# Performance work log

Hardware: AMD Instinct MI355X
Metric: run time of the kernel (lower is better)

The kernel has to match this reference:

```python
import jax, jax.numpy as jnp
import numpy as np

N_NODES = 100000
N_EDGES = 1600000
STATE_DIM = 128
HIDDEN_DIM = 128
ACTION_DIM = 16


def gcn_conv(x, edge_index, W, b, n_nodes):
    """PyG-style GCNConv: add self-loops, symmetric normalization, x@W then aggregate."""
    xw = x @ W  # [N, H]
    loops = jnp.arange(n_nodes, dtype=edge_index.dtype)
    src = jnp.concatenate([edge_index[0], loops])  # [E+N]
    dst = jnp.concatenate([edge_index[1], loops])
    ones = jnp.ones(src.shape[0], dtype=xw.dtype)
    deg = jax.ops.segment_sum(ones, dst, num_segments=n_nodes)  # degree of target nodes
    dinv = jnp.where(deg > 0, jax.lax.rsqrt(deg), 0.0)
    norm = dinv[src] * dinv[dst]  # [E+N]
    msg = xw[src] * norm[:, None]  # gather + scale (irregular access)
    out = jax.ops.segment_sum(msg, dst, num_segments=n_nodes)  # scatter-aggregate
    return out + b


def setup_inputs() -> dict:
    key = jax.random.key(0)
    ks = jax.random.split(key, 12)
    def lin(k, fan_in, shape):
        bound = 1.0 / np.sqrt(fan_in)
        return jax.random.uniform(k, shape, jnp.float32, -bound, bound)
    return {
        "x": jax.random.normal(ks[0], (N_NODES, STATE_DIM), jnp.float32),
        "edge_index": jax.random.randint(ks[1], (2, N_EDGES), 0, N_NODES, jnp.int64),
        "action": jax.random.normal(ks[2], (N_NODES, ACTION_DIM), jnp.float32),
        "gcn1_w": lin(ks[3], STATE_DIM, (STATE_DIM, HIDDEN_DIM)),
        "gcn1_b": lin(ks[4], STATE_DIM, (HIDDEN_DIM,)),
        "gcn2_w": lin(ks[5], HIDDEN_DIM, (HIDDEN_DIM, HIDDEN_DIM)),
        "gcn2_b": lin(ks[6], HIDDEN_DIM, (HIDDEN_DIM,)),
        "fc1_w": lin(ks[7], HIDDEN_DIM + ACTION_DIM, (HIDDEN_DIM + ACTION_DIM, HIDDEN_DIM)),
        "fc1_b": lin(ks[8], HIDDEN_DIM + ACTION_DIM, (HIDDEN_DIM,)),
        "fc2_w": lin(ks[9], HIDDEN_DIM, (HIDDEN_DIM, 1)),
        "fc2_b": lin(ks[10], HIDDEN_DIM, (1,)),
    }


def reference(x, edge_index, action, gcn1_w, gcn1_b, gcn2_w, gcn2_b, fc1_w, fc1_b, fc2_w, fc2_b):
    n = x.shape[0]
    h = jax.nn.relu(gcn_conv(x, edge_index, gcn1_w, gcn1_b, n))
    h = jax.nn.relu(gcn_conv(h, edge_index, gcn2_w, gcn2_b, n))
    h = jnp.concatenate([h, action], axis=-1)  # [N, H+A]
    h = jax.nn.relu(h @ fc1_w + fc1_b)
    q = h @ fc2_w + fc2_b  # [N, 1]
    return q.squeeze(-1)
```

## Files before the change

### kernel.cpp

```cpp
#include <hip/hip_runtime.h>
#include <hip/hip_bf16.h>

typedef unsigned short u16;
typedef unsigned int   u32;
typedef __attribute__((ext_vector_type(8))) short bf16x8;
typedef __attribute__((ext_vector_type(4))) float f32x4;

constexpr int NN = 100000;
constexpr int NE = 1600000;
constexpr int D  = 128;
constexpr size_t WS_NEED = 58909184;

constexpr int NBUCK = 196;
constexpr int NBLKA = 256;
constexpr int EPB   = 6272;
constexpr int CAPA  = 80;

__device__ __forceinline__ float bf2f(u16 u){ union{u32 i;float f;}v; v.i=((u32)u)<<16; return v.f; }
__device__ __forceinline__ float2 bfp(u32 u){ union{u32 i;float f;}a,b; a.i=u<<16; b.i=u&0xffff0000u; return make_float2(a.f,b.f); }
__device__ __forceinline__ u16 f2bf(float f){ union{float f;u32 i;}v; v.f=f; u32 r=v.i + 0x7fffu + ((v.i>>16)&1u); return (u16)(r>>16); }
__device__ __forceinline__ u32 pk2(float a, float b){ return (u32)f2bf(a) | ((u32)f2bf(b)<<16); }

__global__ void detect_kernel(const u32* __restrict__ xw, const int* __restrict__ ei,
                              int* __restrict__ flagf, int* __restrict__ flage){
  __shared__ int shf[256];
  __shared__ int she[256];
  int t = threadIdx.x;
  int cnt = 0;
  for(int i = 0; i < 16; i++){
    u32 w = xw[(t*16 + i) * 256];
    int e = (int)((w >> 7) & 0xFFu);
    cnt += (e >= 64 && e <= 160) ? 1 : 0;
  }
  int nz = 0;
  for(int i = 0; i < 8; i++){
    int k = t*8 + i;
    long long w = 1 + ((long long)k * (2LL*NE - 2)) / 2048;
    nz += (ei[(int)(w | 1)] != 0) ? 1 : 0;
  }
  shf[t] = cnt; she[t] = nz;
  __syncthreads();
  for(int off=128; off>0; off>>=1){
    if(t<off){ shf[t]+=shf[t+off]; she[t]+=she[t+off]; }
    __syncthreads();
  }
  if(t==0){ flagf[0] = (shf[0] < 3000) ? 1 : 0; flage[0] = (she[0] == 0) ? 1 : 0; }
}

__global__ void prep_kernel(const void* __restrict__ w1, const void* __restrict__ w2,
    const void* __restrict__ fw1, const void* __restrict__ b1, const void* __restrict__ b2,
    const void* __restrict__ fb1, const void* __restrict__ fw2, const void* __restrict__ fb2,
    const int* __restrict__ flagf,
    u16* __restrict__ WT1, u16* __restrict__ WT2, u16* __restrict__ WTF, float* __restrict__ BF)
{
  const int ff = flagf[0];
  int i = blockIdx.x*256 + threadIdx.x;
  auto cv = [&](const void* p, int idx)->float{
    return ff ? ((const float*)p)[idx] : bf2f(((const u16*)p)[idx]);
  };
  if(i < 16384){
    int k = i >> 7, d = i & 127;
    WT1[d*128 + k] = f2bf(cv(w1, i));
  }else if(i < 32768){
    int j = i - 16384; int k = j >> 7, d = j & 127;
    WT2[d*128 + k] = f2bf(cv(w2, j));
  }else if(i < 51200){
    int j = i - 32768; int k = j >> 7, d = j & 127;
    WTF[d*144 + k] = f2bf(cv(fw1, j));
  }else if(i < 51713){
    int j = i - 51200;
    if(j < 128)       BF[j]   = cv(b1, j);
    else if(j < 256)  BF[j]   = cv(b2, j-128);
    else if(j < 384)  BF[j]   = cv(fb1, j-256);
    else if(j < 512)  BF[j]   = cv(fw2, j-384);
    else              BF[512] = cv(fb2, 0);
  }
}

__global__ void fill1_kernel(u16* __restrict__ out, int n){
  int i = blockIdx.x*blockDim.x + threadIdx.x;
  if(i < n) out[i] = 0x3F80;
}

__global__ __launch_bounds__(256) void passA_kernel(
    const int* __restrict__ ei, const int* __restrict__ flage,
    u32* __restrict__ ebuf, u32* __restrict__ counts)
{
  __shared__ u32 hist[NBUCK];
  int t = threadIdx.x;
  for(int b = t; b < NBUCK; b += 256) hist[b] = 0;
  __syncthreads();
  const int f = flage[0];
  const int eb = blockIdx.x * EPB;
  const u32 cbase = blockIdx.x * NBUCK;
  for(int i = t; i < EPB; i += 256){
    int e = eb + i;
    if(e >= NE) break;
    int s = f ? ei[2*e]      : ei[e];
    int d = f ? ei[2*(NE+e)] : ei[NE+e];
    if((u32)s >= (u32)NN || (u32)d >= (u32)NN) continue;
    int b = d >> 9;
    u32 rank = atomicAdd(&hist[b], 1u);
    if(rank < CAPA) ebuf[(size_t)(cbase + b)*CAPA + rank] = (u32)s | ((u32)(d & 511) << 17);
  }
  __syncthreads();
  for(int b = t; b < NBUCK; b += 256){
    u32 c = hist[b];
    counts[cbase + b] = (c < CAPA) ? c : CAPA;
  }
}

__global__ void scan196_kernel(const u32* __restrict__ counts, int* __restrict__ bases){
  __shared__ int sh[NBUCK];
  int t = threadIdx.x;
  if(t < NBUCK){
    int tot = 0;
    for(int c = 0; c < NBLKA; c++) tot += counts[c*NBUCK + t];
    sh[t] = tot;
  }
  __syncthreads();
  if(t == 0){
    int acc = 0;
    for(int b = 0; b < NBUCK; b++){ int v = sh[b]; sh[b] = acc; acc += v; }
  }
  __syncthreads();
  if(t < NBUCK) bases[t] = sh[t];
}

__global__ __launch_bounds__(512) void passB_kernel(
    const u32* __restrict__ ebuf, const u32* __restrict__ counts, const int* __restrict__ bases,
    int* __restrict__ deg, int* __restrict__ off, float* __restrict__ dinv,
    int* __restrict__ srcs)
{
  __shared__ int cnt[512];
  __shared__ int nodeoff[512];
  __shared__ int pos[512];
  __shared__ int choff[NBLKA + 1];
  const int t = threadIdx.x;
  const int b = blockIdx.x;
  const int v0 = b << 9;

  cnt[t] = 0;
  __syncthreads();

  if(t < NBLKA) choff[t] = (int)counts[t*NBUCK + b];
  __syncthreads();
  if(t == 0){
    int acc = 0;
    for(int c = 0; c < NBLKA; c++){ int v = choff[c]; choff[c] = acc; acc += v; }
    choff[NBLKA] = acc;
  }
  __syncthreads();
  const int T = choff[NBLKA];

  for(int i = t; i < T; i += 512){
    int lo = 0, hi = NBLKA - 1;
    #pragma unroll
    for(int s = 0; s < 8; s++){
      int mid = (lo + hi) >> 1;
      if(choff[mid + 1] <= i) lo = mid + 1; else hi = mid;
    }
    u32 rec = ebuf[(size_t)(lo*NBUCK + b)*CAPA + (i - choff[lo])];
    atomicAdd(&cnt[rec >> 17], 1);
  }
  __syncthreads();

  int myc = cnt[t];
  nodeoff[t] = myc;
  __syncthreads();
  for(int o = 1; o < 512; o <<= 1){
    int a = (t >= o) ? nodeoff[t - o] : 0;
    __syncthreads();
    nodeoff[t] += a;
    __syncthreads();
  }
  int excl = nodeoff[t] - myc;
  __syncthreads();
  nodeoff[t] = excl;
  pos[t] = 0;
  __syncthreads();

  const int gb = bases[b];

  for(int i = t; i < T; i += 512){
    int lo = 0, hi = NBLKA - 1;
    #pragma unroll
    for(int s = 0; s < 8; s++){
      int mid = (lo + hi) >> 1;
      if(choff[mid + 1] <= i) lo = mid + 1; else hi = mid;
    }
    u32 rec = ebuf[(size_t)(lo*NBUCK + b)*CAPA + (i - choff[lo])];
    int ld = rec >> 17;
    int r = atomicAdd(&pos[ld], 1);
    srcs[gb + nodeoff[ld] + r] = (int)(rec & 0x1FFFFu);
  }

  int v = v0 + t;
  if(v < NN){
    deg[v] = myc;
    off[v] = gb + excl;
    dinv[v] = rsqrtf((float)(myc + 1));
  }
}

template<int K, bool FUSE_Q, bool RAW1, bool RAW2>
__global__ __launch_bounds__(256) void gemm_mfma(
    const void* __restrict__ A1, const void* __restrict__ A2,
    const u16* __restrict__ WT, const float* __restrict__ biasf,
    const float* __restrict__ qwf, const float* __restrict__ qbf,
    const int* __restrict__ flagf, const float* __restrict__ dscale,
    void* __restrict__ out, int n)
{
  constexpr int KT = ((K + 31)/32)*32;
  constexpr int KP = KT + 8;
  __shared__ u16 Ws[128*KP];
  __shared__ u16 As[64*KP];
  const int tid = threadIdx.x;
  const int nb  = blockIdx.x * 64;
  const int ff  = flagf[0];

  constexpr int CPT = KT/8;
  for(int i = tid; i < 128*CPT; i += 256){
    int row = i / CPT, col = (i % CPT) * 8;
    uint4 v = make_uint4(0,0,0,0);
    if(col < K) v = *(const uint4*)(WT + row*K + col);
    *(uint4*)(Ws + row*KP + col) = v;
  }
  for(int i = tid; i < 64*CPT; i += 256){
    int row = i / CPT, col = (i % CPT) * 8;
    int gr = nb + row; if(gr >= n) gr = n-1;
    uint4 v = make_uint4(0,0,0,0);
    if(col < 128){
      if(!RAW1 || !ff){
        v = *(const uint4*)((const u16*)A1 + (size_t)gr*128 + col);
      }else{
        const float* af = (const float*)A1 + (size_t)gr*128 + col;
        float4 p0 = *(const float4*)(af);
        float4 p1 = *(const float4*)(af + 4);
        v.x = pk2(p0.x,p0.y); v.y = pk2(p0.z,p0.w);
        v.z = pk2(p1.x,p1.y); v.w = pk2(p1.z,p1.w);
      }
    }else if(col < K){
      if(!RAW2 || !ff){
        v = *(const uint4*)((const u16*)A2 + (size_t)gr*16 + (col - 128));
      }else{
        const float* af = (const float*)A2 + (size_t)gr*16 + (col - 128);
        float4 p0 = *(const float4*)(af);
        float4 p1 = *(const float4*)(af + 4);
        v.x = pk2(p0.x,p0.y); v.y = pk2(p0.z,p0.w);
        v.z = pk2(p1.x,p1.y); v.w = pk2(p1.z,p1.w);
      }
    }
    *(uint4*)(As + row*KP + col) = v;
  }
  __syncthreads();

  const int wave = tid >> 6;
  const int lane = tid & 63;
  const int quad = lane >> 4;
  const int lm   = lane & 15;

  const u16* Ab = As + (wave*16 + lm)*KP;
  const u16* Bb = Ws + lm*KP;

  f32x4 acc[8];
  #pragma unroll
  for(int t=0;t<8;t++) acc[t] = (f32x4){0.f,0.f,0.f,0.f};

  #pragma unroll
  for(int ki = 0; ki < KT/32; ki++){
    int kk = ki*32 + quad*8;
    bf16x8 a = *(const bf16x8*)(Ab + kk);
    #pragma unroll
    for(int t=0;t<8;t++){
      bf16x8 b = *(const bf16x8*)(Bb + t*16*KP + kk);
      acc[t] = __builtin_amdgcn_mfma_f32_16x16x32_bf16(a, b, acc[t], 0, 0, 0);
    }
  }

  const int node0 = nb + wave*16 + quad*4;
  if(!FUSE_Q){
    #pragma unroll
    for(int r=0;r<4;r++){
      int gr = node0 + r;
      if(gr < n){
        float dv = dscale[gr];
        #pragma unroll
        for(int t=0;t<8;t++){
          ((u16*)out)[(size_t)gr*D + t*16 + lm] = f2bf(acc[t][r]*dv);
        }
      }
    }
  }else{
    float qp[4] = {0.f,0.f,0.f,0.f};
    #pragma unroll
    for(int t=0;t<8;t++){
      float bvt = biasf[t*16 + lm];
      float qwt = qwf[t*16 + lm];
      #pragma unroll
      for(int r=0;r<4;r++){
        float h = fmaxf(acc[t][r] + bvt, 0.f);
        qp[r] += h * qwt;
      }
    }
    #pragma unroll
    for(int r=0;r<4;r++){
      #pragma unroll
      for(int o=1; o<16; o<<=1) qp[r] += __shfl_xor(qp[r], o, 16);
    }
    if(lm == 0){
      float qb = qbf[0];
      #pragma unroll
      for(int r=0;r<4;r++){
        int gr = node0 + r;
        if(gr < n){
          float q = qp[r] + qb;
          if(ff) ((float*)out)[gr] = q;
          else   ((u16*)out)[gr]  = f2bf(q);
        }
      }
    }
  }
}

#define ACC8(r)  { float2 f_;                       \
    f_ = bfp((r).x); a0 += f_.x; a1 += f_.y;        \
    f_ = bfp((r).y); a2 += f_.x; a3 += f_.y;        \
    f_ = bfp((r).z); a4 += f_.x; a5 += f_.y;        \
    f_ = bfp((r).w); a6 += f_.x; a7 += f_.y; }

__global__ __launch_bounds__(256) void gather_kernel(
    const int* __restrict__ off, const int* __restrict__ deg,
    const int* __restrict__ srcs, const float* __restrict__ dinv,
    const u16* __restrict__ xw, const float* __restrict__ biasf,
    u16* __restrict__ h)
{
  const int node = blockIdx.x*16 + (threadIdx.x >> 4);
  const int lane = threadIdx.x & 15;
  const int j0 = off[node];
  const int j1 = j0 + deg[node];

  float a0=0.f,a1=0.f,a2=0.f,a3=0.f,a4=0.f,a5=0.f,a6=0.f,a7=0.f;
  const u16* __restrict__ xl = xw + 8*lane;

  int j = j0;
  int s0=0, s1=0, s2=0, s3=0;
  const bool pre = (j + 4 <= j1);
  if(pre){
    s0 = __builtin_nontemporal_load(&srcs[j]);
    s1 = __builtin_nontemporal_load(&srcs[j+1]);
    s2 = __builtin_nontemporal_load(&srcs[j+2]);
    s3 = __builtin_nontemporal_load(&srcs[j+3]);
  }
  for(; j + 8 <= j1; j += 4){
    uint4 r0 = *(const uint4*)(xl + (size_t)s0*D);
    uint4 r1 = *(const uint4*)(xl + (size_t)s1*D);
    uint4 r2 = *(const uint4*)(xl + (size_t)s2*D);
    uint4 r3 = *(const uint4*)(xl + (size_t)s3*D);
    s0 = __builtin_nontemporal_load(&srcs[j+4]);
    s1 = __builtin_nontemporal_load(&srcs[j+5]);
    s2 = __builtin_nontemporal_load(&srcs[j+6]);
    s3 = __builtin_nontemporal_load(&srcs[j+7]);
    ACC8(r0); ACC8(r1); ACC8(r2); ACC8(r3);
  }
  if(pre){
    uint4 r0 = *(const uint4*)(xl + (size_t)s0*D);
    uint4 r1 = *(const uint4*)(xl + (size_t)s1*D);
    uint4 r2 = *(const uint4*)(xl + (size_t)s2*D);
    uint4 r3 = *(const uint4*)(xl + (size_t)s3*D);
    ACC8(r0); ACC8(r1); ACC8(r2); ACC8(r3);
    j += 4;
  }
  for(; j < j1; j++){
    int s = __builtin_nontemporal_load(&srcs[j]);
    uint4 r = *(const uint4*)(xl + (size_t)s*D);
    ACC8(r);
  }

  uint4 ps = *(const uint4*)(xl + (size_t)node*D);
  ACC8(ps);
  const float dv = dinv[node];
  float4 bA = *(const float4*)(biasf + 8*lane);
  float4 bB = *(const float4*)(biasf + 8*lane + 4);
  float o0 = fmaxf(fmaf(dv,a0,bA.x), 0.f);
  float o1 = fmaxf(fmaf(dv,a1,bA.y), 0.f);
  float o2 = fmaxf(fmaf(dv,a2,bA.z), 0.f);
  float o3 = fmaxf(fmaf(dv,a3,bA.w), 0.f);
  float o4 = fmaxf(fmaf(dv,a4,bB.x), 0.f);
  float o5 = fmaxf(fmaf(dv,a5,bB.y), 0.f);
  float o6 = fmaxf(fmaf(dv,a6,bB.z), 0.f);
  float o7 = fmaxf(fmaf(dv,a7,bB.w), 0.f);
  uint4 pkd;
  pkd.x = pk2(o0,o1); pkd.y = pk2(o2,o3); pkd.z = pk2(o4,o5); pkd.w = pk2(o6,o7);
  *(uint4*)(h + (size_t)node*D + 8*lane) = pkd;
}

extern "C" void kernel_launch(void* const* d_in, const int* in_sizes, int n_in,
                              void* d_out, int out_size, void* d_ws, size_t ws_size,
                              hipStream_t stream)
{
  bool meta_ok = (n_in >= 11) && (in_sizes[0] == NN*D) && (in_sizes[1] == 2*NE)
              && (in_sizes[2] == NN*16) && (out_size == NN);
  if(!meta_ok){
    fill1_kernel<<<(NN+255)/256, 256, 0, stream>>>((u16*)d_out, NN);
    return;
  }
  if(ws_size < WS_NEED) return;

  const void* x      = d_in[0];
  const int*  ei     = (const int*)d_in[1];
  const void* action = d_in[2];
  const void* w1     = d_in[3];
  const void* b1     = d_in[4];
  const void* w2     = d_in[5];
  const void* b2     = d_in[6];
  const void* fw1    = d_in[7];
  const void* fb1    = d_in[8];
  const void* fw2    = d_in[9];
  const void* fb2    = d_in[10];

  char* ws = (char*)d_ws;
  int*   DEG    = (int*)(ws + 0);
  int*   OFF    = (int*)(ws + 400128);
  float* DINV   = (float*)(ws + 800256);
  int*   FLAGE  = (int*)(ws + 1204480);
  int*   FLAGF  = (int*)(ws + 1204544);
  u16*   WT1    = (u16*)(ws + 1204608);
  u16*   WT2    = (u16*)(ws + 1237376);
  u16*   WTF    = (u16*)(ws + 1270144);
  float* BF     = (float*)(ws + 1307008);
  int*   SRCS   = (int*)(ws + 1309184);
  u16*   F0     = (u16*)(ws + 7709184);
  u16*   F1     = (u16*)(ws + 33309184);
  u32*   EBUF   = (u32*)(ws + 33309184);
  u32*   COUNTS = (u32*)(ws + 49365504);
  int*   BASES  = (int*)(ws + 49566208);

  detect_kernel<<<1, 256, 0, stream>>>((const u32*)x, ei, FLAGF, FLAGE);

  passA_kernel<<<NBLKA, 256, 0, stream>>>(ei, FLAGE, EBUF, COUNTS);
  scan196_kernel<<<1, 256, 0, stream>>>(COUNTS, BASES);
  passB_kernel<<<NBUCK, 512, 0, stream>>>(EBUF, COUNTS, BASES, DEG, OFF, DINV, SRCS);

  prep_kernel<<<203, 256, 0, stream>>>(w1, w2, fw1, b1, b2, fb1, fw2, fb2, FLAGF,
                                       WT1, WT2, WTF, BF);

  gemm_mfma<128,false,true,false><<<(NN+63)/64, 256, 0, stream>>>(x, nullptr, WT1, nullptr, nullptr, nullptr, FLAGF, DINV, F0, NN);
  gather_kernel<<<(NN+15)/16, 256, 0, stream>>>(OFF, DEG, SRCS, DINV, F0, BF, F1);

  gemm_mfma<128,false,false,false><<<(NN+63)/64, 256, 0, stream>>>(F1, nullptr, WT2, nullptr, nullptr, nullptr, FLAGF, DINV, F0, NN);
  gather_kernel<<<(NN+15)/16, 256, 0, stream>>>(OFF, DEG, SRCS, DINV, F0, BF+128, F1);

  gemm_mfma<144,true,false,true><<<(NN+63)/64, 256, 0, stream>>>(F1, action, WTF, BF+256, BF+384, BF+512, FLAGF, nullptr, d_out, NN);
}
```

Baseline: 364.2 us.

## Fuse neighbor aggregation with following GEMM per 16-node block

Replaces the separate gather and GEMM kernels for layer 2 and the final MLP with a fused kernel. Each block aggregates 16 nodes into shared memory, then immediately multiplies them by the next weight matrix with MFMA. The final variant also folds in the action concat and the q reduction. This removes the round trip of the hidden activations through global memory and two kernel launches. In exchange, every small block reloads the full weight matrix into LDS, and the larger shared memory footprint reduces occupancy for the latency-bound gather.

Result: no change. 367.5 us (+0.9%).

```diff
diff --git a/kernel.cpp b/kernel.cpp
--- a/kernel.cpp
+++ b/kernel.cpp
@@ -203,145 +203,117 @@
   }
 }
 
-template<int K, bool FUSE_Q, bool RAW1, bool RAW2>
-__global__ __launch_bounds__(256) void gemm_mfma(
-    const void* __restrict__ A1, const void* __restrict__ A2,
-    const u16* __restrict__ WT, const float* __restrict__ biasf,
-    const float* __restrict__ qwf, const float* __restrict__ qbf,
+__global__ __launch_bounds__(256) void gemm1_kernel(
+    const void* __restrict__ A1, const u16* __restrict__ WT,
     const int* __restrict__ flagf, const float* __restrict__ dscale,
-    void* __restrict__ out, int n)
+    u16* __restrict__ out, int n)
 {
-  constexpr int KT = ((K + 31)/32)*32;
-  constexpr int KP = KT + 8;
+  constexpr int KP = 136;
   __shared__ u16 Ws[128*KP];
   __shared__ u16 As[64*KP];
   const int tid = threadIdx.x;
   const int nb  = blockIdx.x * 64;
   const int ff  = flagf[0];
 
+  for(int i = tid; i < 128*16; i += 256){
+    int row = i / 16, col = (i % 16) * 8;
+    *(uint4*)(Ws + row*KP + col) = *(const uint4*)(WT + row*128 + col);
+  }
+  for(int i = tid; i < 64*16; i += 256){
+    int row = i / 16, col = (i % 16) * 8;
+    int gr = nb + row; if(gr >= n) gr = n-1;
+    uint4 v;
+    if(!ff){
+      v = *(const uint4*)((const u16*)A1 + (size_t)gr*128 + col);
+    }else{
+      const float* af = (const float*)A1 + (size_t)gr*128 + col;
+      float4 p0 = *(const float4*)(af);
+      float4 p1 = *(const float4*)(af + 4);
+      v.x = pk2(p0.x,p0.y); v.y = pk2(p0.z,p0.w);
+      v.z = pk2(p1.x,p1.y); v.w = pk2(p1.z,p1.w);
+    }
+    *(uint4*)(As + row*KP + col) = v;
+  }
+  __syncthreads();
+
+  const int wave = tid >> 6;
+  const int lane = tid & 63;
+  const int quad = lane >> 4;
+  const int lm   = lane & 15;
+
+  const u16* Ab = As + (wave*16 + lm)*KP;
+  const u16* Bb = Ws + lm*KP;
+
+  f32x4 acc[8];
+  #pragma unroll
+  for(int t=0;t<8;t++) acc[t] = (f32x4){0.f,0.f,0.f,0.f};
+
+  #pragma unroll
+  for(int ki = 0; ki < 4; ki++){
+    int kk = ki*32 + quad*8;
+    bf16x8 a = *(const bf16x8*)(Ab + kk);
+    #pragma unroll
+    for(int t=0;t<8;t++){
+      bf16x8 b = *(const bf16x8*)(Bb + t*16*KP + kk);
+      acc[t] = __builtin_amdgcn_mfma_f32_16x16x32_bf16(a, b, acc[t], 0, 0, 0);
+    }
+  }
+
+  const int node0 = nb + wave*16 + quad*4;
+  #pragma unroll
+  for(int r=0;r<4;r++){
+    int gr = node0 + r;
+    if(gr < n){
+      float dv = dscale[gr];
+      #pragma unroll
+      for(int t=0;t<8;t++){
+        out[(size_t)gr*D + t*16 + lm] = f2bf(acc[t][r]*dv);
+      }
+    }
+  }
+}
+
+#define ACC8(r)  { float2 f_;                       \
+    f_ = bfp((r).x); a0 += f_.x; a1 += f_.y;        \
+    f_ = bfp((r).y); a2 += f_.x; a3 += f_.y;        \
+    f_ = bfp((r).z); a4 += f_.x; a5 += f_.y;        \
+    f_ = bfp((r).w); a6 += f_.x; a7 += f_.y; }
+
+template<bool FINAL>
+__global__ __launch_bounds__(256) void fused_kernel(
+    const int* __restrict__ off, const int* __restrict__ deg,
+    const int* __restrict__ srcs, const float* __restrict__ dinv,
+    const u16* __restrict__ xw, const float* __restrict__ biasf,
+    const u16* __restrict__ WT, const float* __restrict__ fb1,
+    const float* __restrict__ qwf, const float* __restrict__ qbf,
+    const void* __restrict__ action, const int* __restrict__ flagf,
+    void* __restrict__ out)
+{
+  constexpr int K  = FINAL ? 144 : 128;
+  constexpr int KT = FINAL ? 160 : 128;
+  constexpr int KP = KT + 8;
   constexpr int CPT = KT/8;
+  __shared__ u16 Ws[128*KP];
+  __shared__ u16 Hs[16*KP];
+  __shared__ float qred[FINAL ? 64 : 4];
+
+  const int tid  = threadIdx.x;
+  const int node0 = blockIdx.x * 16;
+  const int nl   = tid >> 4;
+  const int l16  = tid & 15;
+  const int node = node0 + nl;
+
   for(int i = tid; i < 128*CPT; i += 256){
     int row = i / CPT, col = (i % CPT) * 8;
     uint4 v = make_uint4(0,0,0,0);
     if(col < K) v = *(const uint4*)(WT + row*K + col);
     *(uint4*)(Ws + row*KP + col) = v;
   }
-  for(int i = tid; i < 64*CPT; i += 256){
-    int row = i / CPT, col = (i % CPT) * 8;
-    int gr = nb + row; if(gr >= n) gr = n-1;
-    uint4 v = make_uint4(0,0,0,0);
-    if(col < 128){
-      if(!RAW1 || !ff){
-        v = *(const uint4*)((const u16*)A1 + (size_t)gr*128 + col);
-      }else{
-        const float* af = (const float*)A1 + (size_t)gr*128 + col;
-        float4 p0 = *(const float4*)(af);
-        float4 p1 = *(const float4*)(af + 4);
-        v.x = pk2(p0.x,p0.y); v.y = pk2(p0.z,p0.w);
-        v.z = pk2(p1.x,p1.y); v.w = pk2(p1.z,p1.w);
-      }
-    }else if(col < K){
-      if(!RAW2 || !ff){
-        v = *(const uint4*)((const u16*)A2 + (size_t)gr*16 + (col - 128));
-      }else{
-        const float* af = (const float*)A2 + (size_t)gr*16 + (col - 128);
-        float4 p0 = *(const float4*)(af);
-        float4 p1 = *(const float4*)(af + 4);
-        v.x = pk2(p0.x,p0.y); v.y = pk2(p0.z,p0.w);
-        v.z = pk2(p1.x,p1.y); v.w = pk2(p1.z,p1.w);
-      }
-    }
-    *(uint4*)(As + row*KP + col) = v;
-  }
-  __syncthreads();
-
-  const int wave = tid >> 6;
-  const int lane = tid & 63;
-  const int quad = lane >> 4;
-  const int lm   = lane & 15;
-
-  const u16* Ab = As + (wave*16 + lm)*KP;
-  const u16* Bb = Ws + lm*KP;
-
-  f32x4 acc[8];
-  #pragma unroll
-  for(int t=0;t<8;t++) acc[t] = (f32x4){0.f,0.f,0.f,0.f};
-
-  #pragma unroll
-  for(int ki = 0; ki < KT/32; ki++){
-    int kk = ki*32 + quad*8;
-    bf16x8 a = *(const bf16x8*)(Ab + kk);
-    #pragma unroll
-    for(int t=0;t<8;t++){
-      bf16x8 b = *(const bf16x8*)(Bb + t*16*KP + kk);
-      acc[t] = __builtin_amdgcn_mfma_f32_16x16x32_bf16(a, b, acc[t], 0, 0, 0);
-    }
-  }
-
-  const int node0 = nb + wave*16 + quad*4;
-  if(!FUSE_Q){
-    #pragma unroll
-    for(int r=0;r<4;r++){
-      int gr = node0 + r;
-      if(gr < n){
-        float dv = dscale[gr];
-        #pragma unroll
-        for(int t=0;t<8;t++){
-          ((u16*)out)[(size_t)gr*D + t*16 + lm] = f2bf(acc[t][r]*dv);
-        }
-      }
-    }
-  }else{
-    float qp[4] = {0.f,0.f,0.f,0.f};
-    #pragma unroll
-    for(int t=0;t<8;t++){
-      float bvt = biasf[t*16 + lm];
-      float qwt = qwf[t*16 + lm];
-      #pragma unroll
-      for(int r=0;r<4;r++){
-        float h = fmaxf(acc[t][r] + bvt, 0.f);
-        qp[r] += h * qwt;
-      }
-    }
-    #pragma unroll
-    for(int r=0;r<4;r++){
-      #pragma unroll
-      for(int o=1; o<16; o<<=1) qp[r] += __shfl_xor(qp[r], o, 16);
-    }
-    if(lm == 0){
-      float qb = qbf[0];
-      #pragma unroll
-      for(int r=0;r<4;r++){
-        int gr = node0 + r;
-        if(gr < n){
-          float q = qp[r] + qb;
-          if(ff) ((float*)out)[gr] = q;
-          else   ((u16*)out)[gr]  = f2bf(q);
-        }
-      }
-    }
-  }
-}
-
-#define ACC8(r)  { float2 f_;                       \
-    f_ = bfp((r).x); a0 += f_.x; a1 += f_.y;        \
-    f_ = bfp((r).y); a2 += f_.x; a3 += f_.y;        \
-    f_ = bfp((r).z); a4 += f_.x; a5 += f_.y;        \
-    f_ = bfp((r).w); a6 += f_.x; a7 += f_.y; }
-
-__global__ __launch_bounds__(256) void gather_kernel(
-    const int* __restrict__ off, const int* __restrict__ deg,
-    const int* __restrict__ srcs, const float* __restrict__ dinv,
-    const u16* __restrict__ xw, const float* __restrict__ biasf,
-    u16* __restrict__ h)
-{
-  const int node = blockIdx.x*16 + (threadIdx.x >> 4);
-  const int lane = threadIdx.x & 15;
+
   const int j0 = off[node];
   const int j1 = j0 + deg[node];
-
   float a0=0.f,a1=0.f,a2=0.f,a3=0.f,a4=0.f,a5=0.f,a6=0.f,a7=0.f;
-  const u16* __restrict__ xl = xw + 8*lane;
+  const u16* __restrict__ xl = xw + 8*l16;
 
   int j = j0;
   int s0=0, s1=0, s2=0, s3=0;
@@ -380,8 +352,8 @@
   uint4 ps = *(const uint4*)(xl + (size_t)node*D);
   ACC8(ps);
   const float dv = dinv[node];
-  float4 bA = *(const float4*)(biasf + 8*lane);
-  float4 bB = *(const float4*)(biasf + 8*lane + 4);
+  float4 bA = *(const float4*)(biasf + 8*l16);
+  float4 bB = *(const float4*)(biasf + 8*l16 + 4);
   float o0 = fmaxf(fmaf(dv,a0,bA.x), 0.f);
   float o1 = fmaxf(fmaf(dv,a1,bA.y), 0.f);
   float o2 = fmaxf(fmaf(dv,a2,bA.z), 0.f);
@@ -392,7 +364,96 @@
   float o7 = fmaxf(fmaf(dv,a7,bB.w), 0.f);
   uint4 pkd;
   pkd.x = pk2(o0,o1); pkd.y = pk2(o2,o3); pkd.z = pk2(o4,o5); pkd.w = pk2(o6,o7);
-  *(uint4*)(h + (size_t)node*D + 8*lane) = pkd;
+
+  u16* Hp = Hs + nl*KP;
+  *(uint4*)(Hp + 8*l16) = pkd;
+
+  if(FINAL){
+    const int ff = flagf[0];
+    if(ff){
+      if(l16 < 4){
+        const float* af = (const float*)action + (size_t)node*16 + l16*4;
+        float4 p = *(const float4*)af;
+        uint2 q; q.x = pk2(p.x,p.y); q.y = pk2(p.z,p.w);
+        *(uint2*)(Hp + 128 + 4*l16) = q;
+      }
+    }else{
+      if(l16 < 2){
+        uint4 v = *(const uint4*)((const u16*)action + (size_t)node*16 + 8*l16);
+        *(uint4*)(Hp + 128 + 8*l16) = v;
+      }
+    }
+    if(l16 >= 14){
+      *(uint4*)(Hp + 144 + 8*(l16-14)) = make_uint4(0,0,0,0);
+    }
+  }
+  __syncthreads();
+
+  const int wave = tid >> 6;
+  const int lane = tid & 63;
+  const int quad = lane >> 4;
+  const int lm   = lane & 15;
+
+  const u16* Ab = Hs + lm*KP;
+  f32x4 acc[2];
+  acc[0] = (f32x4){0.f,0.f,0.f,0.f};
+  acc[1] = (f32x4){0.f,0.f,0.f,0.f};
+
+  #pragma unroll
+  for(int ki = 0; ki < KT/32; ki++){
+    int kk = ki*32 + quad*8;
+    bf16x8 a = *(const bf16x8*)(Ab + kk);
+    #pragma unroll
+    for(int tt=0; tt<2; tt++){
+      int col0 = (wave*2 + tt)*16;
+      bf16x8 b = *(const bf16x8*)(Ws + (col0 + lm)*KP + kk);
+      acc[tt] = __builtin_amdgcn_mfma_f32_16x16x32_bf16(a, b, acc[tt], 0, 0, 0);
+    }
+  }
+
+  const int rbase = quad*4;
+  if(!FINAL){
+    #pragma unroll
+    for(int r=0;r<4;r++){
+      int gn = node0 + rbase + r;
+      float dvr = dinv[gn];
+      #pragma unroll
+      for(int tt=0;tt<2;tt++){
+        int col = (wave*2 + tt)*16 + lm;
+        ((u16*)out)[(size_t)gn*D + col] = f2bf(acc[tt][r]*dvr);
+      }
+    }
+  }else{
+    float qp[4] = {0.f,0.f,0.f,0.f};
+    #pragma unroll
+    for(int tt=0;tt<2;tt++){
+      int col = (wave*2 + tt)*16 + lm;
+      float bv = fb1[col];
+      float qw = qwf[col];
+      #pragma unroll
+      for(int r=0;r<4;r++){
+        float h = fmaxf(acc[tt][r] + bv, 0.f);
+        qp[r] += h * qw;
+      }
+    }
+    #pragma unroll
+    for(int r=0;r<4;r++){
+      #pragma unroll
+      for(int o=1; o<16; o<<=1) qp[r] += __shfl_xor(qp[r], o, 16);
+    }
+    if(lm == 0){
+      #pragma unroll
+      for(int r=0;r<4;r++) qred[wave*16 + rbase + r] = qp[r];
+    }
+    __syncthreads();
+    if(tid < 16){
+      float q = qred[tid] + qred[16+tid] + qred[32+tid] + qred[48+tid] + qbf[0];
+      int gn = node0 + tid;
+      const int ff = flagf[0];
+      if(ff) ((float*)out)[gn] = q;
+      else   ((u16*)out)[gn]  = f2bf(q);
+    }
+  }
 }
 
 extern "C" void kernel_launch(void* const* d_in, const int* in_sizes, int n_in,
@@ -445,11 +506,11 @@
   prep_kernel<<<203, 256, 0, stream>>>(w1, w2, fw1, b1, b2, fb1, fw2, fb2, FLAGF,
                                        WT1, WT2, WTF, BF);
 
-  gemm_mfma<128,false,true,false><<<(NN+63)/64, 256, 0, stream>>>(x, nullptr, WT1, nullptr, nullptr, nullptr, FLAGF, DINV, F0, NN);
-  gather_kernel<<<(NN+15)/16, 256, 0, stream>>>(OFF, DEG, SRCS, DINV, F0, BF, F1);
-
-  gemm_mfma<128,false,false,false><<<(NN+63)/64, 256, 0, stream>>>(F1, nullptr, WT2, nullptr, nullptr, nullptr, FLAGF, DINV, F0, NN);
-  gather_kernel<<<(NN+15)/16, 256, 0, stream>>>(OFF, DEG, SRCS, DINV, F0, BF+128, F1);
-
-  gemm_mfma<144,true,false,true><<<(NN+63)/64, 256, 0, stream>>>(F1, action, WTF, BF+256, BF+384, BF+512, FLAGF, nullptr, d_out, NN);
-}
+  gemm1_kernel<<<(NN+63)/64, 256, 0, stream>>>(x, WT1, FLAGF, DINV, F0, NN);
+
+  fused_kernel<false><<<(NN+15)/16, 256, 0, stream>>>(
+      OFF, DEG, SRCS, DINV, F0, BF, WT2, nullptr, nullptr, nullptr, nullptr, FLAGF, F1);
+
+  fused_kernel<true><<<(NN+15)/16, 256, 0, stream>>>(
+      OFF, DEG, SRCS, DINV, F1, BF+128, WTF, BF+256, BF+384, BF+512, action, FLAGF, d_out);
+}
```
